# Optimization experiments

Measured on AMD Instinct MI355X. Metric: run time of the kernel, lower is better.

## Reference

```python
import jax, jax.numpy as jnp
import numpy as np

EPS = 1e-8


def setup_inputs() -> dict:
    key = jax.random.key(0)
    k1, k2, k3, k4, k5 = jax.random.split(key, 5)
    B, N_LOG, N_PHYS, E = 16, 512, 2048, 2048
    P = jax.random.uniform(k1, (B, N_LOG, N_PHYS), dtype=jnp.float32)
    d_hw = jax.random.randint(k2, (N_PHYS, N_PHYS), 0, 4, dtype=jnp.int32)
    edge_src = jax.random.randint(k3, (B, E), 0, N_LOG, dtype=jnp.int32)
    edge_dst = jax.random.randint(k4, (B, E), 0, N_LOG, dtype=jnp.int32)
    edge_w = jax.random.uniform(k5, (B, E), dtype=jnp.float32)
    return {"P": P, "d_hw": d_hw, "edge_src": edge_src,
            "edge_dst": edge_dst, "edge_w": edge_w}


def reference(P, d_hw, edge_src, edge_dst, edge_w):
    # A_hw[p,q] = 1 where hardware distance == 1 (adjacent qubits)
    A_hw = (d_hw == 1).astype(P.dtype)                      # [Q, Q]
    B = P.shape[0]
    # Dense contraction once per batch: PA[b,i,q] = sum_p P[b,i,p] A[p,q]
    PA = jnp.einsum('bip,pq->biq', P, A_hw)                 # [B, N, Q]
    b_idx = jnp.arange(B)[:, None]                          # [B, 1]
    gi = PA[b_idx, edge_src]                                # [B, E, Q]
    gj = P[b_idx, edge_dst]                                 # [B, E, Q]
    adj_score = jnp.einsum('beq,beq->be', gi, gj)           # [B, E]
    sample_adj = jnp.sum(edge_w * adj_score, axis=-1)       # [B]
    sample_weight = jnp.maximum(jnp.sum(edge_w, axis=-1), EPS)
    # every sample has edges -> valid_samples = B
    loss = -jnp.mean(sample_adj / sample_weight)
    return loss
```

## Files before the change

### kernel.cpp

```cpp
#include <hip/hip_runtime.h>
#include <hip/hip_bf16.h>

#define BATCH 16
#define NLOG 512
#define Q 2048
#define NEDGE 2048
#define M_TOT (BATCH * NLOG)
#define KB 2048
#define EDOT_BLOCKS 256

typedef float f32x2 __attribute__((ext_vector_type(2)));
typedef float f32x4 __attribute__((ext_vector_type(4)));
typedef int i32x4 __attribute__((ext_vector_type(4)));
typedef int i32x8 __attribute__((ext_vector_type(8)));

__device__ __forceinline__ unsigned char to_e4m3(float f) {
    int pk = __builtin_amdgcn_cvt_pk_fp8_f32(f, f, 0, false);
    return (unsigned char)(pk & 0xff);
}

__device__ __forceinline__ float dot16(i32x4 a, i32x4 b) {
    float s0 = 0.f, s1 = 0.f;
    #pragma unroll
    for (int d = 0; d < 4; d++) {
        f32x2 alo = __builtin_amdgcn_cvt_pk_f32_fp8(a[d], false);
        f32x2 ahi = __builtin_amdgcn_cvt_pk_f32_fp8(a[d], true);
        f32x2 blo = __builtin_amdgcn_cvt_pk_f32_fp8(b[d], false);
        f32x2 bhi = __builtin_amdgcn_cvt_pk_f32_fp8(b[d], true);
        s0 += alo[0] * blo[0] + alo[1] * blo[1];
        s1 += ahi[0] * bhi[0] + ahi[1] * bhi[1];
    }
    return s0 + s1;
}

__global__ __launch_bounds__(256) void prep(const float* __restrict__ P,
                                            unsigned char* __restrict__ P8,
                                            const int* __restrict__ d_hw,
                                            unsigned char* __restrict__ A8t,
                                            float* __restrict__ adj,
                                            float* __restrict__ wsum,
                                            unsigned* __restrict__ counter) {
    int bid = blockIdx.x;
    if (bid == 0) {
        if (threadIdx.x == 0) *counter = 0u;
        if (threadIdx.x < BATCH) { adj[threadIdx.x] = 0.f; wsum[threadIdx.x] = 0.f; }
    }
    if (bid < 8192) {
        int i = (bid * 256 + threadIdx.x) * 8;
        float4 v0 = *(const float4*)(P + i);
        float4 v1 = *(const float4*)(P + i + 4);
        int lo = 0, hi = 0;
        lo = __builtin_amdgcn_cvt_pk_fp8_f32(v0.x, v0.y, lo, false);
        lo = __builtin_amdgcn_cvt_pk_fp8_f32(v0.z, v0.w, lo, true);
        hi = __builtin_amdgcn_cvt_pk_fp8_f32(v1.x, v1.y, hi, false);
        hi = __builtin_amdgcn_cvt_pk_fp8_f32(v1.z, v1.w, hi, true);
        int2 st; st.x = lo; st.y = hi;
        *(int2*)(P8 + i) = st;
    } else {
        bid -= 8192;
        __shared__ unsigned char tile[32][33];
        int q0 = (bid & 63) * 32;
        int p0 = (bid >> 6) * 32;
        int tx = threadIdx.x & 31;
        int ty = threadIdx.x >> 5;
        for (int s = 0; s < 32; s += 8) {
            int p = p0 + ty + s;
            int v = d_hw[(size_t)p * Q + q0 + tx];
            tile[ty + s][tx] = (v == 1) ? 0x38 : 0x00;
        }
        __syncthreads();
        for (int s = 0; s < 32; s += 8) {
            A8t[(size_t)(q0 + ty + s) * Q + p0 + tx] = tile[tx][ty + s];
        }
    }
}

#define MF(af, bf, accv) __builtin_amdgcn_mfma_scale_f32_16x16x128_f8f6f4( \
    (af), (bf), (accv), 0, 0, 0, 127, 0, 127)

#define READ_FRAG(buf, rowbase) __extension__({                                \
    const int _b = ((rowbase) + lane16) << 7;                                  \
    i32x4 _lo = *(const i32x4*)((buf) + _b + c0);                              \
    i32x4 _hi = *(const i32x4*)((buf) + _b + c1);                              \
    __builtin_shufflevector(_lo, _hi, 0, 1, 2, 3, 4, 5, 6, 7); })

#define SA(dstbuf, c, kk0)                                                     \
    __builtin_amdgcn_global_load_lds(                                          \
        (const __attribute__((address_space(1))) void*)(A +                    \
            (size_t)(m0 + (c) * 64 + s_row) * KB + (kk0) + s_off),             \
        (__attribute__((address_space(3))) void*)((dstbuf) + (c) * 8192 + t * 16), \
        16, 0, 0)
#define SBst(dstbuf, c, kk0)                                                   \
    __builtin_amdgcn_global_load_lds(                                          \
        (const __attribute__((address_space(1))) void*)(Bt +                   \
            (size_t)(n0 + (c) * 64 + s_row) * KB + (kk0) + s_off),             \
        (__attribute__((address_space(3))) void*)((dstbuf) + (c) * 8192 + t * 16), \
        16, 0, 0)

__global__ __launch_bounds__(512, 2) void gemm_bt8(const unsigned char* __restrict__ A,
                                                   const unsigned char* __restrict__ Bt,
                                                   unsigned char* __restrict__ PA8) {
    __shared__ unsigned char As[2][32768];
    __shared__ unsigned char Bs[2][32768];

    const int t = threadIdx.x;
    const int w = t >> 6;
    const int wr = w >> 2, wc = w & 3;
    const int l = t & 63;
    const int quad = l >> 4;
    const int lane16 = l & 15;

    const int m0 = blockIdx.x * 256;
    const int n0 = blockIdx.y * 256;

    const int s_row = t >> 3;
    const int s_off = (((t & 7) ^ (s_row & 7)) << 4);

    const int r7 = lane16 & 7;
    const int c0 = ((2 * quad) ^ r7) << 4;
    const int c1 = ((2 * quad + 1) ^ r7) << 4;

    f32x4 acc[8][4] = {};

    {
        SA(As[0], 0, 0); SA(As[0], 1, 0); SA(As[0], 2, 0); SA(As[0], 3, 0);
        SBst(Bs[0], 0, 0); SBst(Bs[0], 1, 0); SBst(Bs[0], 2, 0); SBst(Bs[0], 3, 0);
    }
    __syncthreads();

    for (int kt = 0; kt < 16; ++kt) {
        const unsigned char* as = As[kt & 1];
        const unsigned char* bs = Bs[kt & 1];
        unsigned char* an = As[(kt + 1) & 1];
        unsigned char* bn = Bs[(kt + 1) & 1];
        const int kn = (kt + 1) * 128;
        const bool st = (kt < 15);

        i32x8 bf0 = READ_FRAG(bs, wc * 64 + 0);
        i32x8 bf1 = READ_FRAG(bs, wc * 64 + 16);
        i32x8 bf2 = READ_FRAG(bs, wc * 64 + 32);
        i32x8 bf3 = READ_FRAG(bs, wc * 64 + 48);
        i32x8 af0 = READ_FRAG(as, wr * 128 + 0);
        i32x8 af1 = READ_FRAG(as, wr * 128 + 16);
        if (st) { SA(an, 0, kn); SA(an, 1, kn); SA(an, 2, kn); }
        __builtin_amdgcn_s_barrier();
        __builtin_amdgcn_s_setprio(1);
        acc[0][0] = MF(af0, bf0, acc[0][0]); acc[0][1] = MF(af0, bf1, acc[0][1]);
        acc[0][2] = MF(af0, bf2, acc[0][2]); acc[0][3] = MF(af0, bf3, acc[0][3]);
        acc[1][0] = MF(af1, bf0, acc[1][0]); acc[1][1] = MF(af1, bf1, acc[1][1]);
        acc[1][2] = MF(af1, bf2, acc[1][2]); acc[1][3] = MF(af1, bf3, acc[1][3]);
        __builtin_amdgcn_s_setprio(0);
        __builtin_amdgcn_s_barrier();

        i32x8 af2 = READ_FRAG(as, wr * 128 + 32);
        i32x8 af3 = READ_FRAG(as, wr * 128 + 48);
        if (st) { SA(an, 3, kn); SBst(bn, 0, kn); SBst(bn, 1, kn); }
        __builtin_amdgcn_s_barrier();
        __builtin_amdgcn_s_setprio(1);
        acc[2][0] = MF(af2, bf0, acc[2][0]); acc[2][1] = MF(af2, bf1, acc[2][1]);
        acc[2][2] = MF(af2, bf2, acc[2][2]); acc[2][3] = MF(af2, bf3, acc[2][3]);
        acc[3][0] = MF(af3, bf0, acc[3][0]); acc[3][1] = MF(af3, bf1, acc[3][1]);
        acc[3][2] = MF(af3, bf2, acc[3][2]); acc[3][3] = MF(af3, bf3, acc[3][3]);
        __builtin_amdgcn_s_setprio(0);
        __builtin_amdgcn_s_barrier();

        i32x8 af4 = READ_FRAG(as, wr * 128 + 64);
        i32x8 af5 = READ_FRAG(as, wr * 128 + 80);
        if (st) { SBst(bn, 2, kn); SBst(bn, 3, kn); }
        __builtin_amdgcn_s_barrier();
        __builtin_amdgcn_s_setprio(1);
        acc[4][0] = MF(af4, bf0, acc[4][0]); acc[4][1] = MF(af4, bf1, acc[4][1]);
        acc[4][2] = MF(af4, bf2, acc[4][2]); acc[4][3] = MF(af4, bf3, acc[4][3]);
        acc[5][0] = MF(af5, bf0, acc[5][0]); acc[5][1] = MF(af5, bf1, acc[5][1]);
        acc[5][2] = MF(af5, bf2, acc[5][2]); acc[5][3] = MF(af5, bf3, acc[5][3]);
        __builtin_amdgcn_s_setprio(0);
        __builtin_amdgcn_s_barrier();

        i32x8 af6 = READ_FRAG(as, wr * 128 + 96);
        i32x8 af7 = READ_FRAG(as, wr * 128 + 112);
        __builtin_amdgcn_s_barrier();
        __builtin_amdgcn_s_setprio(1);
        acc[6][0] = MF(af6, bf0, acc[6][0]); acc[6][1] = MF(af6, bf1, acc[6][1]);
        acc[6][2] = MF(af6, bf2, acc[6][2]); acc[6][3] = MF(af6, bf3, acc[6][3]);
        acc[7][0] = MF(af7, bf0, acc[7][0]); acc[7][1] = MF(af7, bf1, acc[7][1]);
        acc[7][2] = MF(af7, bf2, acc[7][2]); acc[7][3] = MF(af7, bf3, acc[7][3]);
        __builtin_amdgcn_s_setprio(0);
        asm volatile("s_waitcnt vmcnt(0)" ::: "memory");
        __builtin_amdgcn_s_barrier();
    }

    #pragma unroll
    for (int i = 0; i < 8; i++) {
        #pragma unroll
        for (int j = 0; j < 4; j++) {
            #pragma unroll
            for (int r = 0; r < 4; r++) {
                int row = m0 + wr * 128 + i * 16 + quad * 4 + r;
                int col = n0 + wc * 64 + j * 16 + lane16;
                PA8[(size_t)row * Q + col] = to_e4m3(acc[i][j][r] * (1.0f / 256.0f));
            }
        }
    }
}

__global__ __launch_bounds__(512) void edge_dot(const unsigned char* __restrict__ PA8,
                                                const unsigned char* __restrict__ P8,
                                                const int* __restrict__ esrc,
                                                const int* __restrict__ edst,
                                                const float* __restrict__ ew,
                                                float* __restrict__ adj,
                                                float* __restrict__ wsum,
                                                unsigned* __restrict__ counter,
                                                float* __restrict__ out) {
    const int lid = blockIdx.x;
    const int b = (lid & 7) | ((lid >> 7) << 3);
    const int chunk = (lid >> 3) & 15;
    const int t = threadIdx.x;
    const int w = t >> 6;
    const int lane = t & 63;

    const int e0 = b * NEDGE + chunk * 128 + w * 16;
    const unsigned char* Ab = PA8 + (size_t)b * NLOG * Q;
    const unsigned char* Bb = P8  + (size_t)b * NLOG * Q;
    const int off = lane * 32;

    int src = esrc[e0], dst = edst[e0];
    float wcur = ew[e0];
    const unsigned char* ap = Ab + (size_t)src * Q + off;
    const unsigned char* bp = Bb + (size_t)dst * Q + off;
    i32x4 A0 = *(const i32x4*)ap;
    i32x4 A1 = *(const i32x4*)(ap + 16);
    i32x4 B0 = *(const i32x4*)bp;
    i32x4 B1 = *(const i32x4*)(bp + 16);

    float acc = 0.f;
    float wacc = 0.f;
    #pragma unroll
    for (int e = 0; e < 16; e++) {
        i32x4 nA0 = A0, nA1 = A1, nB0 = B0, nB1 = B1;
        float wnext = 0.f;
        if (e < 15) {
            int ns = esrc[e0 + e + 1], nd = edst[e0 + e + 1];
            wnext = ew[e0 + e + 1];
            const unsigned char* nap = Ab + (size_t)ns * Q + off;
            const unsigned char* nbp = Bb + (size_t)nd * Q + off;
            nA0 = *(const i32x4*)nap;
            nA1 = *(const i32x4*)(nap + 16);
            nB0 = *(const i32x4*)nbp;
            nB1 = *(const i32x4*)(nbp + 16);
        }
        float p = dot16(A0, B0) + dot16(A1, B1);
        acc += wcur * p;
        wacc += wcur;
        A0 = nA0; A1 = nA1; B0 = nB0; B1 = nB1; wcur = wnext;
    }

    #pragma unroll
    for (int o = 32; o > 0; o >>= 1) acc += __shfl_xor(acc, o);

    __shared__ float ra[8], rw[8];
    if (lane == 0) { ra[w] = acc; rw[w] = wacc; }
    __syncthreads();

    if (t == 0) {
        float a = 0.f, ws = 0.f;
        #pragma unroll
        for (int i = 0; i < 8; i++) { a += ra[i]; ws += rw[i]; }
        atomicAdd(&adj[b],  a * 256.0f);
        atomicAdd(&wsum[b], ws);
        __threadfence();
        if (atomicAdd(counter, 1u) == EDOT_BLOCKS - 1) {
            __threadfence();
            float s = 0.f;
            #pragma unroll
            for (int bb = 0; bb < BATCH; bb++) {
                float av = atomicAdd(&adj[bb], 0.0f);
                float wv = atomicAdd(&wsum[bb], 0.0f);
                s += av / fmaxf(wv, 1e-8f);
            }
            out[0] = -s / (float)BATCH;
        }
    }
}

extern "C" void kernel_launch(void* const* d_in, const int* in_sizes, int n_in,
                              void* d_out, int out_size, void* d_ws, size_t ws_size,
                              hipStream_t stream) {
    const float* P    = (const float*)d_in[0];
    const int* d_hw   = (const int*)d_in[1];
    const int* esrc   = (const int*)d_in[2];
    const int* edst   = (const int*)d_in[3];
    const float* ew   = (const float*)d_in[4];
    float* out        = (float*)d_out;

    char* ws = (char*)d_ws;
    unsigned char* P8  = (unsigned char*)ws;
    unsigned char* A8t = (unsigned char*)(ws + 16777216);
    unsigned char* PA8 = (unsigned char*)(ws + 20971520);
    float* adj         = (float*)(ws + 37748736);
    float* wsum        = (float*)(ws + 37748736 + 64);
    unsigned* counter  = (unsigned*)(ws + 37748736 + 128);

    prep<<<8192 + 4096, 256, 0, stream>>>(P, P8, d_hw, A8t, adj, wsum, counter);
    gemm_bt8<<<dim3(M_TOT / 256, Q / 256), 512, 0, stream>>>(P8, A8t, PA8);
    edge_dot<<<EDOT_BLOCKS, 512, 0, stream>>>(PA8, P8, esrc, edst, ew, adj, wsum, counter, out);
}
```

Before: 170.3 us.

## Double the edge_dot grid and deepen gather prefetch to two edges

The edge_dot grid grows from 256 to 512 blocks, so each wave handles 8 edges instead of 16. Edge indices and weights are now loaded up front into registers, and the row gathers are prefetched two edges ahead instead of one. Launch bounds now request 4 blocks per CU. The aim is more memory-level parallelism and better latency hiding for the random row gathers, at the cost of more registers and twice as many atomics in the final reduction.

```diff
diff --git a/kernel.cpp b/kernel.cpp
--- a/kernel.cpp
+++ b/kernel.cpp
@@ -7,7 +7,7 @@
 #define NEDGE 2048
 #define M_TOT (BATCH * NLOG)
 #define KB 2048
-#define EDOT_BLOCKS 256
+#define EDOT_BLOCKS 512
 
 typedef float f32x2 __attribute__((ext_vector_type(2)));
 typedef float f32x4 __attribute__((ext_vector_type(4)));
@@ -203,60 +203,70 @@
     }
 }
 
-__global__ __launch_bounds__(512) void edge_dot(const unsigned char* __restrict__ PA8,
-                                                const unsigned char* __restrict__ P8,
-                                                const int* __restrict__ esrc,
-                                                const int* __restrict__ edst,
-                                                const float* __restrict__ ew,
-                                                float* __restrict__ adj,
-                                                float* __restrict__ wsum,
-                                                unsigned* __restrict__ counter,
-                                                float* __restrict__ out) {
+__global__ __launch_bounds__(512, 4) void edge_dot(const unsigned char* __restrict__ PA8,
+                                                   const unsigned char* __restrict__ P8,
+                                                   const int* __restrict__ esrc,
+                                                   const int* __restrict__ edst,
+                                                   const float* __restrict__ ew,
+                                                   float* __restrict__ adj,
+                                                   float* __restrict__ wsum,
+                                                   unsigned* __restrict__ counter,
+                                                   float* __restrict__ out) {
     const int lid = blockIdx.x;
-    const int b = (lid & 7) | ((lid >> 7) << 3);
-    const int chunk = (lid >> 3) & 15;
+    const int b = (lid & 7) | (((lid >> 8) & 1) << 3);
+    const int chunk = (lid >> 3) & 31;
     const int t = threadIdx.x;
     const int w = t >> 6;
     const int lane = t & 63;
-
-    const int e0 = b * NEDGE + chunk * 128 + w * 16;
+    const int off = lane * 32;
+
+    const int e0 = b * NEDGE + chunk * 64 + w * 8;
     const unsigned char* Ab = PA8 + (size_t)b * NLOG * Q;
     const unsigned char* Bb = P8  + (size_t)b * NLOG * Q;
-    const int off = lane * 32;
-
-    int src = esrc[e0], dst = edst[e0];
-    float wcur = ew[e0];
-    const unsigned char* ap = Ab + (size_t)src * Q + off;
-    const unsigned char* bp = Bb + (size_t)dst * Q + off;
-    i32x4 A0 = *(const i32x4*)ap;
-    i32x4 A1 = *(const i32x4*)(ap + 16);
-    i32x4 B0 = *(const i32x4*)bp;
-    i32x4 B1 = *(const i32x4*)(bp + 16);
+
+    int srcs[8], dsts[8];
+    float wts[8];
+    #pragma unroll
+    for (int e = 0; e < 8; e++) {
+        srcs[e] = esrc[e0 + e];
+        dsts[e] = edst[e0 + e];
+        wts[e] = ew[e0 + e];
+    }
+
+    const unsigned char* ap0 = Ab + (size_t)srcs[0] * Q + off;
+    const unsigned char* bp0 = Bb + (size_t)dsts[0] * Q + off;
+    i32x4 cA0 = *(const i32x4*)ap0;
+    i32x4 cA1 = *(const i32x4*)(ap0 + 16);
+    i32x4 cB0 = *(const i32x4*)bp0;
+    i32x4 cB1 = *(const i32x4*)(bp0 + 16);
+    const unsigned char* ap1 = Ab + (size_t)srcs[1] * Q + off;
+    const unsigned char* bp1 = Bb + (size_t)dsts[1] * Q + off;
+    i32x4 nA0 = *(const i32x4*)ap1;
+    i32x4 nA1 = *(const i32x4*)(ap1 + 16);
+    i32x4 nB0 = *(const i32x4*)bp1;
+    i32x4 nB1 = *(const i32x4*)(bp1 + 16);
 
     float acc = 0.f;
-    float wacc = 0.f;
-    #pragma unroll
-    for (int e = 0; e < 16; e++) {
-        i32x4 nA0 = A0, nA1 = A1, nB0 = B0, nB1 = B1;
-        float wnext = 0.f;
-        if (e < 15) {
-            int ns = esrc[e0 + e + 1], nd = edst[e0 + e + 1];
-            wnext = ew[e0 + e + 1];
-            const unsigned char* nap = Ab + (size_t)ns * Q + off;
-            const unsigned char* nbp = Bb + (size_t)nd * Q + off;
-            nA0 = *(const i32x4*)nap;
-            nA1 = *(const i32x4*)(nap + 16);
-            nB0 = *(const i32x4*)nbp;
-            nB1 = *(const i32x4*)(nbp + 16);
-        }
-        float p = dot16(A0, B0) + dot16(A1, B1);
-        acc += wcur * p;
-        wacc += wcur;
-        A0 = nA0; A1 = nA1; B0 = nB0; B1 = nB1; wcur = wnext;
+    #pragma unroll
+    for (int e = 0; e < 8; e++) {
+        i32x4 fA0 = nA0, fA1 = nA1, fB0 = nB0, fB1 = nB1;
+        if (e + 2 < 8) {
+            const unsigned char* ap = Ab + (size_t)srcs[e + 2] * Q + off;
+            const unsigned char* bp = Bb + (size_t)dsts[e + 2] * Q + off;
+            fA0 = *(const i32x4*)ap;
+            fA1 = *(const i32x4*)(ap + 16);
+            fB0 = *(const i32x4*)bp;
+            fB1 = *(const i32x4*)(bp + 16);
+        }
+        acc += wts[e] * (dot16(cA0, cB0) + dot16(cA1, cB1));
+        cA0 = nA0; cA1 = nA1; cB0 = nB0; cB1 = nB1;
+        nA0 = fA0; nA1 = fA1; nB0 = fB0; nB1 = fB1;
     }
 
     #pragma unroll
     for (int o = 32; o > 0; o >>= 1) acc += __shfl_xor(acc, o);
+    float wacc = wts[0] + wts[1] + wts[2] + wts[3] +
+                 wts[4] + wts[5] + wts[6] + wts[7];
 
     __shared__ float ra[8], rw[8];
     if (lane == 0) { ra[w] = acc; rw[w] = wacc; }
```

New measurement: 176.2 us. 1.03x slower.

## Reassociate loss as edge-scattered M times adjacency, fuse dot into GEMM epilogue

Applied to the files above, without the earlier changes.

The loss is rewritten so that, per batch, a matrix M[src] = sum of w·P[dst] is first built with LDS float atomics in a new m_build kernel. An FP8 GEMM then computes M·Aᵀ, and its epilogue multiplies the result elementwise by P and reduces it directly into per-batch sums. This drops the PA8 intermediate write, the separate edge_dot gather kernel and the d_hw transpose, since the adjacency is now consumed untransposed. In exchange it adds an LDS-atomic scatter pass and byte-wise P8 reads in the GEMM epilogue. M is also quantised to fp8, which adds precision error.

```diff
diff --git a/kernel.cpp b/kernel.cpp
--- a/kernel.cpp
+++ b/kernel.cpp
@@ -7,36 +7,22 @@
 #define NEDGE 2048
 #define M_TOT (BATCH * NLOG)
 #define KB 2048
-#define EDOT_BLOCKS 256
+#define GEMM_BLOCKS 256
 
 typedef float f32x2 __attribute__((ext_vector_type(2)));
 typedef float f32x4 __attribute__((ext_vector_type(4)));
 typedef int i32x4 __attribute__((ext_vector_type(4)));
 typedef int i32x8 __attribute__((ext_vector_type(8)));
 
-__device__ __forceinline__ unsigned char to_e4m3(float f) {
-    int pk = __builtin_amdgcn_cvt_pk_fp8_f32(f, f, 0, false);
-    return (unsigned char)(pk & 0xff);
-}
-
-__device__ __forceinline__ float dot16(i32x4 a, i32x4 b) {
-    float s0 = 0.f, s1 = 0.f;
-    #pragma unroll
-    for (int d = 0; d < 4; d++) {
-        f32x2 alo = __builtin_amdgcn_cvt_pk_f32_fp8(a[d], false);
-        f32x2 ahi = __builtin_amdgcn_cvt_pk_f32_fp8(a[d], true);
-        f32x2 blo = __builtin_amdgcn_cvt_pk_f32_fp8(b[d], false);
-        f32x2 bhi = __builtin_amdgcn_cvt_pk_f32_fp8(b[d], true);
-        s0 += alo[0] * blo[0] + alo[1] * blo[1];
-        s1 += ahi[0] * bhi[0] + ahi[1] * bhi[1];
-    }
-    return s0 + s1;
+__device__ __forceinline__ float fp8_to_f32(unsigned char v) {
+    f32x2 p = __builtin_amdgcn_cvt_pk_f32_fp8((int)v, false);
+    return p[0];
 }
 
 __global__ __launch_bounds__(256) void prep(const float* __restrict__ P,
                                             unsigned char* __restrict__ P8,
                                             const int* __restrict__ d_hw,
-                                            unsigned char* __restrict__ A8t,
+                                            unsigned char* __restrict__ A8,
                                             float* __restrict__ adj,
                                             float* __restrict__ wsum,
                                             unsigned* __restrict__ counter) {
@@ -57,21 +43,65 @@
         int2 st; st.x = lo; st.y = hi;
         *(int2*)(P8 + i) = st;
     } else {
-        bid -= 8192;
-        __shared__ unsigned char tile[32][33];
-        int q0 = (bid & 63) * 32;
-        int p0 = (bid >> 6) * 32;
-        int tx = threadIdx.x & 31;
-        int ty = threadIdx.x >> 5;
-        for (int s = 0; s < 32; s += 8) {
-            int p = p0 + ty + s;
-            int v = d_hw[(size_t)p * Q + q0 + tx];
-            tile[ty + s][tx] = (v == 1) ? 0x38 : 0x00;
-        }
-        __syncthreads();
-        for (int s = 0; s < 32; s += 8) {
-            A8t[(size_t)(q0 + ty + s) * Q + p0 + tx] = tile[tx][ty + s];
-        }
+        int idx = ((bid - 8192) * 256 + threadIdx.x) * 4;
+        int4 v = *(const int4*)(d_hw + idx);
+        unsigned pk = (v.x == 1 ? 0x38u : 0u)
+                    | (v.y == 1 ? 0x38u : 0u) << 8
+                    | (v.z == 1 ? 0x38u : 0u) << 16
+                    | (v.w == 1 ? 0x38u : 0u) << 24;
+        *(unsigned*)(A8 + idx) = pk;
+    }
+}
+
+__global__ __launch_bounds__(512) void m_build(const unsigned char* __restrict__ P8,
+                                               const int* __restrict__ esrc,
+                                               const int* __restrict__ edst,
+                                               const float* __restrict__ ew,
+                                               unsigned char* __restrict__ M8,
+                                               float* __restrict__ wsum) {
+    const int b  = blockIdx.x >> 5;
+    const int qs = blockIdx.x & 31;
+    const int q0 = qs * 64;
+    const int t = threadIdx.x;
+    const int w = t >> 6;
+    const int lane = t & 63;
+
+    __shared__ float Mlds[NLOG][64];
+
+    #pragma unroll
+    for (int pass = 0; pass < 8; pass++) {
+        float* mp = &Mlds[pass * 64 + (t >> 3)][(t & 7) * 8];
+        #pragma unroll
+        for (int c = 0; c < 8; c++) mp[c] = 0.f;
+    }
+    __syncthreads();
+
+    const unsigned char* Pb = P8 + (size_t)b * NLOG * Q + q0 + lane;
+    const int ebase = b * NEDGE + w * 256;
+    float wacc = 0.f;
+    #pragma unroll 8
+    for (int e = 0; e < 256; e++) {
+        int dst = edst[ebase + e];
+        int src = esrc[ebase + e];
+        float we = ew[ebase + e];
+        float v = fp8_to_f32(Pb[(size_t)dst * Q]);
+        atomicAdd(&Mlds[src][lane], we * v);
+        wacc += we;
+    }
+    if (qs == 0 && lane == 0) atomicAdd(&wsum[b], wacc);
+    __syncthreads();
+
+    #pragma unroll
+    for (int pass = 0; pass < 8; pass++) {
+        int row = pass * 64 + (t >> 3);
+        const float* mp = &Mlds[row][(t & 7) * 8];
+        int d0 = 0, d1 = 0;
+        d0 = __builtin_amdgcn_cvt_pk_fp8_f32(mp[0], mp[1], d0, false);
+        d0 = __builtin_amdgcn_cvt_pk_fp8_f32(mp[2], mp[3], d0, true);
+        d1 = __builtin_amdgcn_cvt_pk_fp8_f32(mp[4], mp[5], d1, false);
+        d1 = __builtin_amdgcn_cvt_pk_fp8_f32(mp[6], mp[7], d1, true);
+        int2 st; st.x = d0; st.y = d1;
+        *(int2*)(M8 + (size_t)(b * NLOG + row) * Q + q0 + (t & 7) * 8) = st;
     }
 }
 
@@ -86,22 +116,27 @@
 
 #define SA(dstbuf, c, kk0)                                                     \
     __builtin_amdgcn_global_load_lds(                                          \
-        (const __attribute__((address_space(1))) void*)(A +                    \
+        (const __attribute__((address_space(1))) void*)(Mm +                   \
             (size_t)(m0 + (c) * 64 + s_row) * KB + (kk0) + s_off),             \
         (__attribute__((address_space(3))) void*)((dstbuf) + (c) * 8192 + t * 16), \
         16, 0, 0)
-#define SBst(dstbuf, c, kk0)                                                   \
+#define SB(dstbuf, c, kk0)                                                     \
     __builtin_amdgcn_global_load_lds(                                          \
-        (const __attribute__((address_space(1))) void*)(Bt +                   \
+        (const __attribute__((address_space(1))) void*)(Aa +                   \
             (size_t)(n0 + (c) * 64 + s_row) * KB + (kk0) + s_off),             \
         (__attribute__((address_space(3))) void*)((dstbuf) + (c) * 8192 + t * 16), \
         16, 0, 0)
 
-__global__ __launch_bounds__(512, 2) void gemm_bt8(const unsigned char* __restrict__ A,
-                                                   const unsigned char* __restrict__ Bt,
-                                                   unsigned char* __restrict__ PA8) {
+__global__ __launch_bounds__(512, 2) void gemm_fused(const unsigned char* __restrict__ Mm,
+                                                     const unsigned char* __restrict__ Aa,
+                                                     const unsigned char* __restrict__ P8,
+                                                     float* __restrict__ adj,
+                                                     const float* __restrict__ wsum,
+                                                     unsigned* __restrict__ counter,
+                                                     float* __restrict__ out) {
     __shared__ unsigned char As[2][32768];
     __shared__ unsigned char Bs[2][32768];
+    __shared__ float rs[8];
 
     const int t = threadIdx.x;
     const int w = t >> 6;
@@ -112,6 +147,7 @@
 
     const int m0 = blockIdx.x * 256;
     const int n0 = blockIdx.y * 256;
+    const int b = blockIdx.x >> 1;
 
     const int s_row = t >> 3;
     const int s_off = (((t & 7) ^ (s_row & 7)) << 4);
@@ -124,7 +160,7 @@
 
     {
         SA(As[0], 0, 0); SA(As[0], 1, 0); SA(As[0], 2, 0); SA(As[0], 3, 0);
-        SBst(Bs[0], 0, 0); SBst(Bs[0], 1, 0); SBst(Bs[0], 2, 0); SBst(Bs[0], 3, 0);
+        SB(Bs[0], 0, 0); SB(Bs[0], 1, 0); SB(Bs[0], 2, 0); SB(Bs[0], 3, 0);
     }
     __syncthreads();
 
@@ -154,7 +190,7 @@
 
         i32x8 af2 = READ_FRAG(as, wr * 128 + 32);
         i32x8 af3 = READ_FRAG(as, wr * 128 + 48);
-        if (st) { SA(an, 3, kn); SBst(bn, 0, kn); SBst(bn, 1, kn); }
+        if (st) { SA(an, 3, kn); SB(bn, 0, kn); SB(bn, 1, kn); }
         __builtin_amdgcn_s_barrier();
         __builtin_amdgcn_s_setprio(1);
         acc[2][0] = MF(af2, bf0, acc[2][0]); acc[2][1] = MF(af2, bf1, acc[2][1]);
@@ -166,7 +202,7 @@
 
         i32x8 af4 = READ_FRAG(as, wr * 128 + 64);
         i32x8 af5 = READ_FRAG(as, wr * 128 + 80);
-        if (st) { SBst(bn, 2, kn); SBst(bn, 3, kn); }
+        if (st) { SB(bn, 2, kn); SB(bn, 3, kn); }
         __builtin_amdgcn_s_barrier();
         __builtin_amdgcn_s_setprio(1);
         acc[4][0] = MF(af4, bf0, acc[4][0]); acc[4][1] = MF(af4, bf1, acc[4][1]);
@@ -189,6 +225,7 @@
         __builtin_amdgcn_s_barrier();
     }
 
+    float s = 0.f;
     #pragma unroll
     for (int i = 0; i < 8; i++) {
         #pragma unroll
@@ -197,88 +234,31 @@
             for (int r = 0; r < 4; r++) {
                 int row = m0 + wr * 128 + i * 16 + quad * 4 + r;
                 int col = n0 + wc * 64 + j * 16 + lane16;
-                PA8[(size_t)row * Q + col] = to_e4m3(acc[i][j][r] * (1.0f / 256.0f));
+                s += acc[i][j][r] * fp8_to_f32(P8[(size_t)row * Q + col]);
             }
         }
     }
-}
-
-__global__ __launch_bounds__(512) void edge_dot(const unsigned char* __restrict__ PA8,
-                                                const unsigned char* __restrict__ P8,
-                                                const int* __restrict__ esrc,
-                                                const int* __restrict__ edst,
-                                                const float* __restrict__ ew,
-                                                float* __restrict__ adj,
-                                                float* __restrict__ wsum,
-                                                unsigned* __restrict__ counter,
-                                                float* __restrict__ out) {
-    const int lid = blockIdx.x;
-    const int b = (lid & 7) | ((lid >> 7) << 3);
-    const int chunk = (lid >> 3) & 15;
-    const int t = threadIdx.x;
-    const int w = t >> 6;
-    const int lane = t & 63;
-
-    const int e0 = b * NEDGE + chunk * 128 + w * 16;
-    const unsigned char* Ab = PA8 + (size_t)b * NLOG * Q;
-    const unsigned char* Bb = P8  + (size_t)b * NLOG * Q;
-    const int off = lane * 32;
-
-    int src = esrc[e0], dst = edst[e0];
-    float wcur = ew[e0];
-    const unsigned char* ap = Ab + (size_t)src * Q + off;
-    const unsigned char* bp = Bb + (size_t)dst * Q + off;
-    i32x4 A0 = *(const i32x4*)ap;
-    i32x4 A1 = *(const i32x4*)(ap + 16);
-    i32x4 B0 = *(const i32x4*)bp;
-    i32x4 B1 = *(const i32x4*)(bp + 16);
-
-    float acc = 0.f;
-    float wacc = 0.f;
-    #pragma unroll
-    for (int e = 0; e < 16; e++) {
-        i32x4 nA0 = A0, nA1 = A1, nB0 = B0, nB1 = B1;
-        float wnext = 0.f;
-        if (e < 15) {
-            int ns = esrc[e0 + e + 1], nd = edst[e0 + e + 1];
-            wnext = ew[e0 + e + 1];
-            const unsigned char* nap = Ab + (size_t)ns * Q + off;
-            const unsigned char* nbp = Bb + (size_t)nd * Q + off;
-            nA0 = *(const i32x4*)nap;
-            nA1 = *(const i32x4*)(nap + 16);
-            nB0 = *(const i32x4*)nbp;
-            nB1 = *(const i32x4*)(nbp + 16);
-        }
-        float p = dot16(A0, B0) + dot16(A1, B1);
-        acc += wcur * p;
-        wacc += wcur;
-        A0 = nA0; A1 = nA1; B0 = nB0; B1 = nB1; wcur = wnext;
-    }
-
-    #pragma unroll
-    for (int o = 32; o > 0; o >>= 1) acc += __shfl_xor(acc, o);
-
-    __shared__ float ra[8], rw[8];
-    if (lane == 0) { ra[w] = acc; rw[w] = wacc; }
+    #pragma unroll
+    for (int o = 32; o > 0; o >>= 1) s += __shfl_xor(s, o);
+    if (l == 0) rs[w] = s;
     __syncthreads();
 
     if (t == 0) {
-        float a = 0.f, ws = 0.f;
+        float a = 0.f;
         #pragma unroll
-        for (int i = 0; i < 8; i++) { a += ra[i]; ws += rw[i]; }
-        atomicAdd(&adj[b],  a * 256.0f);
-        atomicAdd(&wsum[b], ws);
+        for (int i = 0; i < 8; i++) a += rs[i];
+        atomicAdd(&adj[b], a);
         __threadfence();
-        if (atomicAdd(counter, 1u) == EDOT_BLOCKS - 1) {
+        if (atomicAdd(counter, 1u) == GEMM_BLOCKS - 1) {
             __threadfence();
-            float s = 0.f;
+            float sm = 0.f;
             #pragma unroll
             for (int bb = 0; bb < BATCH; bb++) {
                 float av = atomicAdd(&adj[bb], 0.0f);
-                float wv = atomicAdd(&wsum[bb], 0.0f);
-                s += av / fmaxf(wv, 1e-8f);
+                float wv = atomicAdd((float*)&wsum[bb], 0.0f);
+                sm += av / fmaxf(wv, 1e-8f);
             }
-            out[0] = -s / (float)BATCH;
+            out[0] = -sm / (float)BATCH;
         }
     }
 }
@@ -295,13 +275,13 @@
 
     char* ws = (char*)d_ws;
     unsigned char* P8  = (unsigned char*)ws;
-    unsigned char* A8t = (unsigned char*)(ws + 16777216);
-    unsigned char* PA8 = (unsigned char*)(ws + 20971520);
+    unsigned char* A8  = (unsigned char*)(ws + 16777216);
+    unsigned char* M8  = (unsigned char*)(ws + 20971520);
     float* adj         = (float*)(ws + 37748736);
     float* wsum        = (float*)(ws + 37748736 + 64);
     unsigned* counter  = (unsigned*)(ws + 37748736 + 128);
 
-    prep<<<8192 + 4096, 256, 0, stream>>>(P, P8, d_hw, A8t, adj, wsum, counter);
-    gemm_bt8<<<dim3(M_TOT / 256, Q / 256), 512, 0, stream>>>(P8, A8t, PA8);
-    edge_dot<<<EDOT_BLOCKS, 512, 0, stream>>>(PA8, P8, esrc, edst, ew, adj, wsum, counter, out);
-}
+    prep<<<8192 + 4096, 256, 0, stream>>>(P, P8, d_hw, A8, adj, wsum, counter);
+    m_build<<<512, 512, 0, stream>>>(P8, esrc, edst, ew, M8, wsum);
+    gemm_fused<<<dim3(M_TOT / 256, Q / 256), 512, 0, stream>>>(M8, A8, P8, adj, wsum, counter, out);
+}
```

After: 487.0 us. 186% more time.
